# Performance work log

Hardware: AMD Instinct MI355X
Metric: run time of the kernel (lower is better)

## Reference

```python
import jax, jax.numpy as jnp
import numpy as np

N = 50000   # nodes
E = 800000  # edges
IN, HID, HEADS, OUT = 128, 32, 4, 64
NEG_SLOPE = 0.2


def _gatv2_layer(x, src, dst, Wl, bl, Wr, br, att, bias, res_W, concat):
    """One PyG-style GATv2Conv layer (eval mode, no dropout).
    x: [N, F_in]; att: [H, C]. Returns [N, H*C] if concat else [N, C]."""
    H, C = att.shape
    xl = (x @ Wl + bl).reshape(N, H, C)   # source transform
    xr = (x @ Wr + br).reshape(N, H, C)   # target transform
    e = jax.nn.leaky_relu(xl[src] + xr[dst], NEG_SLOPE)        # [E, H, C]
    logit = jnp.einsum('ehc,hc->eh', e, att)                   # [E, H]
    # segment softmax over incoming edges per destination node
    m = jax.ops.segment_max(logit, dst, num_segments=N)        # [N, H]
    p = jnp.exp(logit - m[dst])
    denom = jax.ops.segment_sum(p, dst, num_segments=N)
    alpha = p / (denom[dst] + 1e-16)                           # [E, H]
    out = jax.ops.segment_sum(xl[src] * alpha[:, :, None], dst, num_segments=N)  # [N, H, C]
    out = out.reshape(N, H * C) if concat else out.mean(axis=1)
    if res_W is not None:
        out = out + x @ res_W
    return out + bias


def _glorot(key, shape):
    fan_in = shape[0] if len(shape) > 1 else shape[-1]
    return jax.random.normal(key, shape, dtype=jnp.float32) / np.sqrt(fan_in)


def setup_inputs() -> dict:
    key = jax.random.key(0)
    ks = iter(jax.random.split(key, 32))
    x = jax.random.normal(next(ks), (N, IN), dtype=jnp.float32)
    edge_index = jax.random.randint(next(ks), (2, E), 0, N, dtype=jnp.int64)
    d = {"x": x, "edge_index": edge_index}
    HC = HEADS * HID  # 128
    # layer 0: IN -> HEADS*HID, concat, residual
    d["Wl0"] = _glorot(next(ks), (IN, HC)); d["bl0"] = jnp.zeros((HC,), jnp.float32)
    d["Wr0"] = _glorot(next(ks), (IN, HC)); d["br0"] = jnp.zeros((HC,), jnp.float32)
    d["att0"] = _glorot(next(ks), (HEADS, HID)); d["b0"] = jnp.zeros((HC,), jnp.float32)
    d["res0"] = _glorot(next(ks), (IN, HC))
    # layer 1: HC -> HEADS*HID, concat, residual
    d["Wl1"] = _glorot(next(ks), (HC, HC)); d["bl1"] = jnp.zeros((HC,), jnp.float32)
    d["Wr1"] = _glorot(next(ks), (HC, HC)); d["br1"] = jnp.zeros((HC,), jnp.float32)
    d["att1"] = _glorot(next(ks), (HEADS, HID)); d["b1"] = jnp.zeros((HC,), jnp.float32)
    d["res1"] = _glorot(next(ks), (HC, HC))
    # layer 2: HC -> OUT, heads=1, concat=False, no residual
    d["Wl2"] = _glorot(next(ks), (HC, OUT)); d["bl2"] = jnp.zeros((OUT,), jnp.float32)
    d["Wr2"] = _glorot(next(ks), (HC, OUT)); d["br2"] = jnp.zeros((OUT,), jnp.float32)
    d["att2"] = _glorot(next(ks), (1, OUT)); d["b2"] = jnp.zeros((OUT,), jnp.float32)
    return d


def reference(x, edge_index,
              Wl0, bl0, Wr0, br0, att0, b0, res0,
              Wl1, bl1, Wr1, br1, att1, b1, res1,
              Wl2, bl2, Wr2, br2, att2, b2):
    src, dst = edge_index[0], edge_index[1]
    h = _gatv2_layer(x, src, dst, Wl0, bl0, Wr0, br0, att0, b0, res0, True)
    h = jax.nn.elu(h)
    h = _gatv2_layer(h, src, dst, Wl1, bl1, Wr1, br1, att1, b1, res1, True)
    h = jax.nn.elu(h)
    return _gatv2_layer(h, src, dst, Wl2, bl2, Wr2, br2, att2, b2, None, False)
```

## Files before the change

kernel.cpp:

```cpp
#include <hip/hip_runtime.h>
#include <math.h>

#define NN 50000
#define EE 800000
#define NBK 196
#define EPB 4096

typedef short v8s __attribute__((ext_vector_type(8)));
typedef float v4f __attribute__((ext_vector_type(4)));
typedef float v16f __attribute__((ext_vector_type(16)));

__device__ __forceinline__ ushort f2bf(float f) {
    uint u = __float_as_uint(f);
    uint r = (u + 0x7fffu + ((u >> 16) & 1u)) >> 16;
    return (ushort)r;
}
__device__ __forceinline__ float bf2f(ushort h) {
    return __uint_as_float(((uint)h) << 16);
}
__device__ __forceinline__ float lrelu(float x) {
    return fmaf(0.4f, fabsf(x), 0.6f * x);
}

template <int CTRL>
__device__ __forceinline__ float dppadd(float x) {
    int y = __builtin_amdgcn_update_dpp(0, __float_as_int(x), CTRL, 0xf, 0xf, true);
    return x + __int_as_float(y);
}
__device__ __forceinline__ float sum8(float x) {
    x = dppadd<0xB1>(x);
    x = dppadd<0x4E>(x);
    x = dppadd<0x141>(x);
    return x;
}
__device__ __forceinline__ float sum16(float x) {
    x = sum8(x);
    x = dppadd<0x140>(x);
    return x;
}
__device__ __forceinline__ float expclamp(float t) {
    return __expf(fminf(fmaxf(t, -60.f), 80.f));
}

__global__ __launch_bounds__(256) void k_bktcnt(const int* __restrict__ edst,
                                                int* __restrict__ bcnt) {
    __shared__ int h[NBK];
    int t = threadIdx.x;
    if (t < NBK) h[t] = 0;
    __syncthreads();
    int eb = blockIdx.x * EPB;
    #pragma unroll
    for (int k = 0; k < EPB / 256; ++k) {
        int e = eb + k * 256 + t;
        if (e < EE) atomicAdd(&h[edst[e] >> 8], 1);
    }
    __syncthreads();
    if (t < NBK && h[t]) atomicAdd(&bcnt[t], h[t]);
}

__global__ __launch_bounds__(256) void k_bscan(const int* __restrict__ bcnt,
                                               int* __restrict__ bbase,
                                               int* __restrict__ bcur) {
    __shared__ int sm[256];
    int t = threadIdx.x;
    int v = (t < NBK) ? bcnt[t] : 0;
    sm[t] = v;
    __syncthreads();
    for (int o = 1; o < 256; o <<= 1) {
        int a = (t >= o) ? sm[t - o] : 0;
        __syncthreads();
        sm[t] += a;
        __syncthreads();
    }
    if (t < NBK) { int ex = sm[t] - v; bbase[t] = ex; bcur[t] = ex; }
}

__global__ __launch_bounds__(256) void k_bktplace(const int* __restrict__ esrc,
                                                  const int* __restrict__ edst,
                                                  int* __restrict__ bcur,
                                                  uint* __restrict__ ebuf) {
    __shared__ int h[NBK];
    __shared__ int base[NBK];
    int t = threadIdx.x;
    if (t < NBK) h[t] = 0;
    __syncthreads();
    int eb = blockIdx.x * EPB;
    int pk[EPB / 256];
    #pragma unroll
    for (int k = 0; k < EPB / 256; ++k) {
        int e = eb + k * 256 + t;
        pk[k] = -1;
        if (e < EE) {
            int b = edst[e] >> 8;
            int r = atomicAdd(&h[b], 1);
            pk[k] = (b << 16) | r;
        }
    }
    __syncthreads();
    if (t < NBK && h[t]) base[t] = atomicAdd(&bcur[t], h[t]);
    __syncthreads();
    #pragma unroll
    for (int k = 0; k < EPB / 256; ++k) {
        int e = eb + k * 256 + t;
        if (e < EE) {
            int b = pk[k] >> 16;
            int r = pk[k] & 0xFFFF;
            uint dl = (uint)(edst[e] & 255);
            ebuf[base[b] + r] = (dl << 16) | (uint)esrc[e];
        }
    }
}

__global__ __launch_bounds__(256) void k_bktfin(const uint* __restrict__ ebuf,
                                                const int* __restrict__ bbase,
                                                const int* __restrict__ bcnt,
                                                int* __restrict__ rowptr,
                                                int* __restrict__ csrc) {
    __shared__ int deg[256];
    __shared__ int sm[256];
    __shared__ int cur[256];
    const int b = blockIdx.x;
    const int t = threadIdx.x;
    const int eb = bbase[b];
    const int ec = bcnt[b];
    deg[t] = 0;
    __syncthreads();
    for (int k = t; k < ec; k += 256)
        atomicAdd(&deg[ebuf[eb + k] >> 16], 1);
    __syncthreads();
    int v = deg[t];
    sm[t] = v;
    __syncthreads();
    for (int o = 1; o < 256; o <<= 1) {
        int a = (t >= o) ? sm[t - o] : 0;
        __syncthreads();
        sm[t] += a;
        __syncthreads();
    }
    int node = b * 256 + t;
    if (node < NN) rowptr[node + 1] = eb + sm[t];
    if (node == 0) rowptr[0] = 0;
    cur[t] = sm[t] - v;
    __syncthreads();
    for (int k = t; k < ec; k += 256) {
        uint u = ebuf[eb + k];
        int nl = (int)(u >> 16);
        int r = atomicAdd(&cur[nl], 1);
        csrc[eb + r] = (int)(u & 0xFFFFu);
    }
}

struct WPack {
    const float* W[8];
    ushort* Th[8];
    ushort* Tl[8];
    int fout[8];
};

__global__ __launch_bounds__(256) void k_conv_w(WPack p) {
    int wi = blockIdx.y;
    int fout = p.fout[wi];
    int total = 128 * fout;
    int i = blockIdx.x * 256 + threadIdx.x;
    if (i >= total) return;
    int k = i / fout;
    int n = i - k * fout;
    float f = p.W[wi][i];
    ushort h = f2bf(f);
    float lo = f - bf2f(h);
    int t = n >> 5, c32 = n & 31, c = k >> 4, khalf = (k >> 3) & 1, j = k & 7;
    int flat = (((t * 8 + c) * 64) + khalf * 32 + c32) * 8 + j;
    p.Th[wi][flat] = h;
    p.Tl[wi][flat] = f2bf(lo);
}

template <int FOUT, int NW, bool CVT>
__global__ __launch_bounds__(128) void k_gemm_mfma(
    const float* __restrict__ Xf,
    const ushort* __restrict__ Xh, const ushort* __restrict__ Xl,
    const ushort* __restrict__ T0h, const ushort* __restrict__ T0l, const float* __restrict__ B0,
    const ushort* __restrict__ T1h, const ushort* __restrict__ T1l, const float* __restrict__ B1,
    const ushort* __restrict__ T2h, const ushort* __restrict__ T2l,
    ushort* __restrict__ O0b, float* __restrict__ O1, float* __restrict__ O2)
{
    const int lane  = threadIdx.x & 63;
    const int wid   = threadIdx.x >> 6;
    const int c32   = lane & 31;
    const int khalf = lane >> 5;
    const int row0  = blockIdx.x * 64 + wid * 32;

    const ushort* Th[3] = {T0h, T1h, T2h};
    const ushort* Tl[3] = {T0l, T1l, T2l};
    const float*  Bp[3] = {B0, B1, nullptr};

    v8s ah[8], al[8];
    {
        int arow = row0 + c32;
        if (arow > NN - 1) arow = NN - 1;
        #pragma unroll
        for (int c = 0; c < 8; ++c) {
            size_t off = (size_t)arow * 128 + c * 16 + khalf * 8;
            if constexpr (CVT) {
                float4 f0 = *(const float4*)(Xf + off);
                float4 f1 = *(const float4*)(Xf + off + 4);
                const float fe[8] = {f0.x, f0.y, f0.z, f0.w, f1.x, f1.y, f1.z, f1.w};
                #pragma unroll
                for (int e = 0; e < 8; ++e) {
                    ushort h = f2bf(fe[e]);
                    float lo = fe[e] - bf2f(h);
                    ah[c][e] = (short)h;
                    al[c][e] = (short)(__float_as_uint(lo) >> 16);
                }
            } else {
                ah[c] = *(const v8s*)(Xh + off);
                al[c] = *(const v8s*)(Xl + off);
            }
        }
    }

    #pragma unroll
    for (int w = 0; w < NW; ++w) {
        const ushort* th = Th[w];
        const ushort* tl = Tl[w];
        const float* bias = Bp[w];
        float* Of = (w == 1) ? O1 : O2;
        #pragma unroll
        for (int t = 0; t < FOUT / 32; ++t) {
            v16f acc = {0.f,0.f,0.f,0.f, 0.f,0.f,0.f,0.f, 0.f,0.f,0.f,0.f, 0.f,0.f,0.f,0.f};
            #pragma unroll
            for (int c = 0; c < 8; ++c) {
                int boff = ((t * 8 + c) * 64 + lane) * 8;
                v8s bh = *(const v8s*)(th + boff);
                v8s bl = *(const v8s*)(tl + boff);
                acc = __builtin_amdgcn_mfma_f32_32x32x16_bf16(al[c], bh, acc, 0, 0, 0);
                acc = __builtin_amdgcn_mfma_f32_32x32x16_bf16(ah[c], bl, acc, 0, 0, 0);
                acc = __builtin_amdgcn_mfma_f32_32x32x16_bf16(ah[c], bh, acc, 0, 0, 0);
            }
            const int col = t * 32 + c32;
            float badd = bias ? bias[col] : 0.f;
            if (w == 0) {
                #pragma unroll
                for (int reg = 0; reg < 16; ++reg) {
                    int r = row0 + (reg & 3) + 8 * (reg >> 2) + 4 * khalf;
                    if (r < NN) O0b[(size_t)r * FOUT + col] = f2bf(acc[reg] + badd);
                }
            } else {
                #pragma unroll
                for (int reg = 0; reg < 16; ++reg) {
                    int r = row0 + (reg & 3) + 8 * (reg >> 2) + 4 * khalf;
                    if (r < NN) Of[(size_t)r * FOUT + col] = acc[reg] + badd;
                }
            }
        }
    }
}

__global__ __launch_bounds__(256) void k_agg01(const ushort* __restrict__ XLb,
                                               const float4* __restrict__ XR4,
                                               const float4* __restrict__ RES4,
                                               const float* __restrict__ att,
                                               const float* __restrict__ bias,
                                               const int* __restrict__ rowptr,
                                               const int* __restrict__ csrc,
                                               ushort* __restrict__ Hh,
                                               ushort* __restrict__ Hl) {
    const int lane = threadIdx.x & 63;
    const int wid = threadIdx.x >> 6;
    const int n = blockIdx.x * 4 + wid;
    if (n >= NN) return;
    const int beg = rowptr[n];
    const int end = rowptr[n + 1];
    const int half = lane >> 5;
    const uint j = lane & 31;

    const float4 xr = XR4[(uint)n * 32u + j];
    const float4 at = ((const float4*)att)[j];
    float4 s = {0.f, 0.f, 0.f, 0.f};
    float d = 0.f;

    int i = beg;
    for (; i + 4 <= end; i += 4) {
        uint sa = (uint)csrc[i + half];
        uint sb = (uint)csrc[i + 2 + half];
        ushort4 ua = *(const ushort4*)(XLb + sa * 128u + 4u * j);
        ushort4 ub = *(const ushort4*)(XLb + sb * 128u + 4u * j);
        {
            float4 va = {bf2f(ua.x), bf2f(ua.y), bf2f(ua.z), bf2f(ua.w)};
            float t0 = lrelu(va.x + xr.x) * at.x;
            t0 = fmaf(lrelu(va.y + xr.y), at.y, t0);
            t0 = fmaf(lrelu(va.z + xr.z), at.z, t0);
            t0 = fmaf(lrelu(va.w + xr.w), at.w, t0);
            float p = expclamp(sum8(t0));
            d += p;
            s.x = fmaf(p, va.x, s.x); s.y = fmaf(p, va.y, s.y);
            s.z = fmaf(p, va.z, s.z); s.w = fmaf(p, va.w, s.w);
        }
        {
            float4 vb = {bf2f(ub.x), bf2f(ub.y), bf2f(ub.z), bf2f(ub.w)};
            float t0 = lrelu(vb.x + xr.x) * at.x;
            t0 = fmaf(lrelu(vb.y + xr.y), at.y, t0);
            t0 = fmaf(lrelu(vb.z + xr.z), at.z, t0);
            t0 = fmaf(lrelu(vb.w + xr.w), at.w, t0);
            float p = expclamp(sum8(t0));
            d += p;
            s.x = fmaf(p, vb.x, s.x); s.y = fmaf(p, vb.y, s.y);
            s.z = fmaf(p, vb.z, s.z); s.w = fmaf(p, vb.w, s.w);
        }
    }
    for (; i < end; i += 2) {
        int ia = i + half;
        if (ia > end - 1) ia = end - 1;
        uint sa = (uint)csrc[ia];
        ushort4 ua = *(const ushort4*)(XLb + sa * 128u + 4u * j);
        float4 va = {bf2f(ua.x), bf2f(ua.y), bf2f(ua.z), bf2f(ua.w)};
        float t0 = lrelu(va.x + xr.x) * at.x;
        t0 = fmaf(lrelu(va.y + xr.y), at.y, t0);
        t0 = fmaf(lrelu(va.z + xr.z), at.z, t0);
        t0 = fmaf(lrelu(va.w + xr.w), at.w, t0);
        float p = expclamp(sum8(t0));
        if (half && (i + 1 >= end)) p = 0.f;
        d += p;
        s.x = fmaf(p, va.x, s.x); s.y = fmaf(p, va.y, s.y);
        s.z = fmaf(p, va.z, s.z); s.w = fmaf(p, va.w, s.w);
    }

    d   += __shfl_xor(d, 32);
    s.x += __shfl_xor(s.x, 32);
    s.y += __shfl_xor(s.y, 32);
    s.z += __shfl_xor(s.z, 32);
    s.w += __shfl_xor(s.w, 32);

    if (half == 0) {
        float inv = (d > 0.f) ? 1.f / d : 0.f;
        float4 rv = RES4[(uint)n * 32u + j];
        float4 bv = ((const float4*)bias)[j];
        float o0 = fmaf(s.x, inv, rv.x + bv.x);
        float o1 = fmaf(s.y, inv, rv.y + bv.y);
        float o2 = fmaf(s.z, inv, rv.z + bv.z);
        float o3 = fmaf(s.w, inv, rv.w + bv.w);
        o0 = o0 > 0.f ? o0 : __expf(o0) - 1.f;
        o1 = o1 > 0.f ? o1 : __expf(o1) - 1.f;
        o2 = o2 > 0.f ? o2 : __expf(o2) - 1.f;
        o3 = o3 > 0.f ? o3 : __expf(o3) - 1.f;
        ushort4 h, l;
        h.x = f2bf(o0); l.x = f2bf(o0 - bf2f(h.x));
        h.y = f2bf(o1); l.y = f2bf(o1 - bf2f(h.y));
        h.z = f2bf(o2); l.z = f2bf(o2 - bf2f(h.z));
        h.w = f2bf(o3); l.w = f2bf(o3 - bf2f(h.w));
        *(ushort4*)(Hh + (uint)n * 128u + 4u * j) = h;
        *(ushort4*)(Hl + (uint)n * 128u + 4u * j) = l;
    }
}

__global__ __launch_bounds__(256) void k_agg2(const ushort* __restrict__ XLb,
                                              const float4* __restrict__ XR4,
                                              const float* __restrict__ att,
                                              const float* __restrict__ bias,
                                              const int* __restrict__ rowptr,
                                              const int* __restrict__ csrc,
                                              float* __restrict__ OUT) {
    const int lane = threadIdx.x & 63;
    const int wid = threadIdx.x >> 6;
    const int n = blockIdx.x * 4 + wid;
    if (n >= NN) return;
    const int beg = rowptr[n];
    const int end = rowptr[n + 1];
    const int q = lane >> 4;
    const uint jj = lane & 15;

    const float4 xr = XR4[(uint)n * 16u + jj];
    const float4 at = ((const float4*)att)[jj];
    float4 s = {0.f, 0.f, 0.f, 0.f};
    float d = 0.f;
    const int e1 = end - 1;

    for (int i = beg; i < end; i += 8) {
        int i0 = i + q;
        int i1 = i + 4 + q;
        uint s0 = (uint)csrc[min(i0, e1)];
        uint s1 = (uint)csrc[min(i1, e1)];
        ushort4 u0 = *(const ushort4*)(XLb + s0 * 64u + 4u * jj);
        ushort4 u1 = *(const ushort4*)(XLb + s1 * 64u + 4u * jj);
        #pragma unroll
        for (int u = 0; u < 2; ++u) {
            ushort4 uv = (u == 0) ? u0 : u1;
            int ii = (u == 0) ? i0 : i1;
            float4 v = {bf2f(uv.x), bf2f(uv.y), bf2f(uv.z), bf2f(uv.w)};
            float t0 = lrelu(v.x + xr.x) * at.x;
            t0 = fmaf(lrelu(v.y + xr.y), at.y, t0);
            t0 = fmaf(lrelu(v.z + xr.z), at.z, t0);
            t0 = fmaf(lrelu(v.w + xr.w), at.w, t0);
            float p = expclamp(sum16(t0));
            if (ii >= end) p = 0.f;
            d += p;
            s.x = fmaf(p, v.x, s.x); s.y = fmaf(p, v.y, s.y);
            s.z = fmaf(p, v.z, s.z); s.w = fmaf(p, v.w, s.w);
        }
    }

    d   += __shfl_xor(d, 16);   d   += __shfl_xor(d, 32);
    s.x += __shfl_xor(s.x, 16); s.x += __shfl_xor(s.x, 32);
    s.y += __shfl_xor(s.y, 16); s.y += __shfl_xor(s.y, 32);
    s.z += __shfl_xor(s.z, 16); s.z += __shfl_xor(s.z, 32);
    s.w += __shfl_xor(s.w, 16); s.w += __shfl_xor(s.w, 32);

    if (lane < 16) {
        float inv = (d > 0.f) ? 1.f / d : 0.f;
        float4 bv = ((const float4*)bias)[jj];
        float4 o;
        o.x = fmaf(s.x, inv, bv.x);
        o.y = fmaf(s.y, inv, bv.y);
        o.z = fmaf(s.z, inv, bv.z);
        o.w = fmaf(s.w, inv, bv.w);
        *(float4*)(OUT + (uint)n * 64u + 4u * jj) = o;
    }
}

extern "C" void kernel_launch(void* const* d_in, const int* in_sizes, int n_in,
                              void* d_out, int out_size, void* d_ws, size_t ws_size,
                              hipStream_t stream) {
    const float* x    = (const float*)d_in[0];
    const int*   ei   = (const int*)d_in[1];
    const int*   esrc = ei;
    const int*   edst = ei + EE;

    const float* Wl0 = (const float*)d_in[2];
    const float* bl0 = (const float*)d_in[3];
    const float* Wr0 = (const float*)d_in[4];
    const float* br0 = (const float*)d_in[5];
    const float* at0 = (const float*)d_in[6];
    const float* b0  = (const float*)d_in[7];
    const float* rs0 = (const float*)d_in[8];
    const float* Wl1 = (const float*)d_in[9];
    const float* bl1 = (const float*)d_in[10];
    const float* Wr1 = (const float*)d_in[11];
    const float* br1 = (const float*)d_in[12];
    const float* at1 = (const float*)d_in[13];
    const float* b1  = (const float*)d_in[14];
    const float* rs1 = (const float*)d_in[15];
    const float* Wl2 = (const float*)d_in[16];
    const float* bl2 = (const float*)d_in[17];
    const float* Wr2 = (const float*)d_in[18];
    const float* br2 = (const float*)d_in[19];
    const float* at2 = (const float*)d_in[20];
    const float* b2  = (const float*)d_in[21];

    float* out = (float*)d_out;

    ushort* XLb = (ushort*)d_ws;
    float* XR  = (float*)(XLb + (size_t)NN * 128);
    float* RES = XR + (size_t)NN * 128;
    ushort* Xh = (ushort*)(RES + (size_t)NN * 128);
    ushort* Xl_ = Xh + (size_t)NN * 128;
    ushort* Wth = Xl_ + (size_t)NN * 128;
    const int wsz[8] = {16384, 16384, 16384, 16384, 16384, 16384, 8192, 8192};
    ushort* th[8]; ushort* tl[8];
    {
        ushort* p = Wth;
        for (int i = 0; i < 8; ++i) { th[i] = p; p += wsz[i]; }
        for (int i = 0; i < 8; ++i) { tl[i] = p; p += wsz[i]; }
    }
    int* bcnt   = (int*)(Wth + 2 * (6 * 16384 + 2 * 8192));
    int* bbase  = bcnt + 256;
    int* bcur   = bbase + 256;
    int* rowptr = bcur + 256;
    int* csrc   = rowptr + (NN + 1);
    uint* ebuf  = (uint*)(csrc + EE);

    hipMemsetAsync(bcnt, 0, 256 * sizeof(int), stream);
    const int ebk = (EE + EPB - 1) / EPB;
    k_bktcnt<<<ebk, 256, 0, stream>>>(edst, bcnt);
    k_bscan<<<1, 256, 0, stream>>>(bcnt, bbase, bcur);
    k_bktplace<<<ebk, 256, 0, stream>>>(esrc, edst, bcur, ebuf);
    k_bktfin<<<NBK, 256, 0, stream>>>(ebuf, bbase, bcnt, rowptr, csrc);

    WPack wp;
    const float* Ws[8] = {Wl0, Wr0, rs0, Wl1, Wr1, rs1, Wl2, Wr2};
    const int fouts[8] = {128, 128, 128, 128, 128, 128, 64, 64};
    for (int i = 0; i < 8; ++i) { wp.W[i] = Ws[i]; wp.Th[i] = th[i]; wp.Tl[i] = tl[i]; wp.fout[i] = fouts[i]; }
    k_conv_w<<<dim3(64, 8), 256, 0, stream>>>(wp);

    const int gemm_gx = (NN + 63) / 64;
    const int agg_grid = (NN + 3) / 4;

    k_gemm_mfma<128, 3, true><<<gemm_gx, 128, 0, stream>>>(x, nullptr, nullptr,
        th[0], tl[0], bl0, th[1], tl[1], br0, th[2], tl[2], XLb, XR, RES);
    k_agg01<<<agg_grid, 256, 0, stream>>>(XLb, (const float4*)XR, (const float4*)RES,
        at0, b0, rowptr, csrc, Xh, Xl_);

    k_gemm_mfma<128, 3, false><<<gemm_gx, 128, 0, stream>>>(nullptr, Xh, Xl_,
        th[3], tl[3], bl1, th[4], tl[4], br1, th[5], tl[5], XLb, XR, RES);
    k_agg01<<<agg_grid, 256, 0, stream>>>(XLb, (const float4*)XR, (const float4*)RES,
        at1, b1, rowptr, csrc, Xh, Xl_);

    k_gemm_mfma<64, 2, false><<<gemm_gx, 128, 0, stream>>>(nullptr, Xh, Xl_,
        th[6], tl[6], bl2, th[7], tl[7], br2, nullptr, nullptr, XLb, XR, nullptr);
    k_agg2<<<agg_grid, 256, 0, stream>>>(XLb, (const float4*)XR, at2, b2, rowptr, csrc, out);
}
```

Before: 381.4 us.

## Fuse CSR build launches with weight conversion and shrink GEMM blocks to one wave

Merges the bucket-count kernel and the weight bf16 split-conversion into one launch, and removes the separate scan kernel. Each place and finalize block now recomputes the 196-entry bucket prefix scan itself. This cuts the preprocessing chain from five launches to three and removes serialization between them, at the cost of redundant scan work in every block. The GEMM kernels also switch to 64-thread blocks covering 32 rows each, doubling the grid, for finer scheduling granularity.

```diff
diff --git a/kernel.cpp b/kernel.cpp
--- a/kernel.cpp
+++ b/kernel.cpp
@@ -42,48 +42,71 @@
     return __expf(fminf(fmaxf(t, -60.f), 80.f));
 }
 
-__global__ __launch_bounds__(256) void k_bktcnt(const int* __restrict__ edst,
-                                                int* __restrict__ bcnt) {
-    __shared__ int h[NBK];
+struct WPack {
+    const float* W[8];
+    ushort* Th[8];
+    ushort* Tl[8];
+    int fout[8];
+};
+
+__global__ __launch_bounds__(256) void k_build1(const int* __restrict__ edst,
+                                                int* __restrict__ bcnt,
+                                                WPack p) {
     int t = threadIdx.x;
-    if (t < NBK) h[t] = 0;
-    __syncthreads();
-    int eb = blockIdx.x * EPB;
-    #pragma unroll
-    for (int k = 0; k < EPB / 256; ++k) {
-        int e = eb + k * 256 + t;
-        if (e < EE) atomicAdd(&h[edst[e] >> 8], 1);
-    }
-    __syncthreads();
-    if (t < NBK && h[t]) atomicAdd(&bcnt[t], h[t]);
-}
-
-__global__ __launch_bounds__(256) void k_bscan(const int* __restrict__ bcnt,
-                                               int* __restrict__ bbase,
-                                               int* __restrict__ bcur) {
-    __shared__ int sm[256];
-    int t = threadIdx.x;
-    int v = (t < NBK) ? bcnt[t] : 0;
-    sm[t] = v;
-    __syncthreads();
-    for (int o = 1; o < 256; o <<= 1) {
-        int a = (t >= o) ? sm[t - o] : 0;
-        __syncthreads();
-        sm[t] += a;
-        __syncthreads();
-    }
-    if (t < NBK) { int ex = sm[t] - v; bbase[t] = ex; bcur[t] = ex; }
+    if (blockIdx.x < 196) {
+        __shared__ int h[NBK];
+        if (t < NBK) h[t] = 0;
+        __syncthreads();
+        int eb = blockIdx.x * EPB;
+        #pragma unroll
+        for (int k = 0; k < EPB / 256; ++k) {
+            int e = eb + k * 256 + t;
+            if (e < EE) atomicAdd(&h[edst[e] >> 8], 1);
+        }
+        __syncthreads();
+        if (t < NBK && h[t]) atomicAdd(&bcnt[t], h[t]);
+    } else {
+        int bid = blockIdx.x - 196;
+        int wi = bid >> 6;
+        int ib = bid & 63;
+        int fout = p.fout[wi];
+        int total = 128 * fout;
+        int i = ib * 256 + t;
+        if (i >= total) return;
+        int k = i / fout;
+        int n = i - k * fout;
+        float f = p.W[wi][i];
+        ushort h = f2bf(f);
+        float lo = f - bf2f(h);
+        int tt = n >> 5, c32 = n & 31, c = k >> 4, khalf = (k >> 3) & 1, j = k & 7;
+        int flat = (((tt * 8 + c) * 64) + khalf * 32 + c32) * 8 + j;
+        p.Th[wi][flat] = h;
+        p.Tl[wi][flat] = f2bf(lo);
+    }
 }
 
 __global__ __launch_bounds__(256) void k_bktplace(const int* __restrict__ esrc,
                                                   const int* __restrict__ edst,
-                                                  int* __restrict__ bcur,
+                                                  const int* __restrict__ bcnt,
+                                                  int* __restrict__ gcur,
                                                   uint* __restrict__ ebuf) {
+    __shared__ int sc[256];
     __shared__ int h[NBK];
     __shared__ int base[NBK];
     int t = threadIdx.x;
+    int v = (t < NBK) ? bcnt[t] : 0;
+    sc[t] = v;
+    __syncthreads();
+    for (int o = 1; o < 256; o <<= 1) {
+        int a = (t >= o) ? sc[t - o] : 0;
+        __syncthreads();
+        sc[t] += a;
+        __syncthreads();
+    }
+    int bexcl = sc[t] - v;
     if (t < NBK) h[t] = 0;
     __syncthreads();
+
     int eb = blockIdx.x * EPB;
     int pk[EPB / 256];
     #pragma unroll
@@ -97,7 +120,7 @@
         }
     }
     __syncthreads();
-    if (t < NBK && h[t]) base[t] = atomicAdd(&bcur[t], h[t]);
+    if (t < NBK && h[t]) base[t] = bexcl + atomicAdd(&gcur[t], h[t]);
     __syncthreads();
     #pragma unroll
     for (int k = 0; k < EPB / 256; ++k) {
@@ -112,24 +135,36 @@
 }
 
 __global__ __launch_bounds__(256) void k_bktfin(const uint* __restrict__ ebuf,
-                                                const int* __restrict__ bbase,
                                                 const int* __restrict__ bcnt,
                                                 int* __restrict__ rowptr,
                                                 int* __restrict__ csrc) {
+    __shared__ int sm[256];
     __shared__ int deg[256];
-    __shared__ int sm[256];
     __shared__ int cur[256];
+    __shared__ int s_eb, s_ec;
     const int b = blockIdx.x;
     const int t = threadIdx.x;
-    const int eb = bbase[b];
-    const int ec = bcnt[b];
+
+    int v = (t < NBK) ? bcnt[t] : 0;
+    sm[t] = v;
     deg[t] = 0;
     __syncthreads();
+    for (int o = 1; o < 256; o <<= 1) {
+        int a = (t >= o) ? sm[t - o] : 0;
+        __syncthreads();
+        sm[t] += a;
+        __syncthreads();
+    }
+    if (t == b) { s_eb = sm[t] - v; s_ec = v; }
+    __syncthreads();
+    const int eb = s_eb;
+    const int ec = s_ec;
+
     for (int k = t; k < ec; k += 256)
         atomicAdd(&deg[ebuf[eb + k] >> 16], 1);
     __syncthreads();
-    int v = deg[t];
-    sm[t] = v;
+    int dv = deg[t];
+    sm[t] = dv;
     __syncthreads();
     for (int o = 1; o < 256; o <<= 1) {
         int a = (t >= o) ? sm[t - o] : 0;
@@ -140,7 +175,7 @@
     int node = b * 256 + t;
     if (node < NN) rowptr[node + 1] = eb + sm[t];
     if (node == 0) rowptr[0] = 0;
-    cur[t] = sm[t] - v;
+    cur[t] = sm[t] - dv;
     __syncthreads();
     for (int k = t; k < ec; k += 256) {
         uint u = ebuf[eb + k];
@@ -150,32 +185,8 @@
     }
 }
 
-struct WPack {
-    const float* W[8];
-    ushort* Th[8];
-    ushort* Tl[8];
-    int fout[8];
-};
-
-__global__ __launch_bounds__(256) void k_conv_w(WPack p) {
-    int wi = blockIdx.y;
-    int fout = p.fout[wi];
-    int total = 128 * fout;
-    int i = blockIdx.x * 256 + threadIdx.x;
-    if (i >= total) return;
-    int k = i / fout;
-    int n = i - k * fout;
-    float f = p.W[wi][i];
-    ushort h = f2bf(f);
-    float lo = f - bf2f(h);
-    int t = n >> 5, c32 = n & 31, c = k >> 4, khalf = (k >> 3) & 1, j = k & 7;
-    int flat = (((t * 8 + c) * 64) + khalf * 32 + c32) * 8 + j;
-    p.Th[wi][flat] = h;
-    p.Tl[wi][flat] = f2bf(lo);
-}
-
 template <int FOUT, int NW, bool CVT>
-__global__ __launch_bounds__(128) void k_gemm_mfma(
+__global__ __launch_bounds__(64) void k_gemm_mfma(
     const float* __restrict__ Xf,
     const ushort* __restrict__ Xh, const ushort* __restrict__ Xl,
     const ushort* __restrict__ T0h, const ushort* __restrict__ T0l, const float* __restrict__ B0,
@@ -184,10 +195,9 @@
     ushort* __restrict__ O0b, float* __restrict__ O1, float* __restrict__ O2)
 {
     const int lane  = threadIdx.x & 63;
-    const int wid   = threadIdx.x >> 6;
     const int c32   = lane & 31;
     const int khalf = lane >> 5;
-    const int row0  = blockIdx.x * 64 + wid * 32;
+    const int row0  = blockIdx.x * 32;
 
     const ushort* Th[3] = {T0h, T1h, T2h};
     const ushort* Tl[3] = {T0l, T1l, T2l};
@@ -461,39 +471,35 @@
         for (int i = 0; i < 8; ++i) { tl[i] = p; p += wsz[i]; }
     }
     int* bcnt   = (int*)(Wth + 2 * (6 * 16384 + 2 * 8192));
-    int* bbase  = bcnt + 256;
-    int* bcur   = bbase + 256;
-    int* rowptr = bcur + 256;
+    int* gcur   = bcnt + 256;
+    int* rowptr = gcur + 256;
     int* csrc   = rowptr + (NN + 1);
     uint* ebuf  = (uint*)(csrc + EE);
-
-    hipMemsetAsync(bcnt, 0, 256 * sizeof(int), stream);
-    const int ebk = (EE + EPB - 1) / EPB;
-    k_bktcnt<<<ebk, 256, 0, stream>>>(edst, bcnt);
-    k_bscan<<<1, 256, 0, stream>>>(bcnt, bbase, bcur);
-    k_bktplace<<<ebk, 256, 0, stream>>>(esrc, edst, bcur, ebuf);
-    k_bktfin<<<NBK, 256, 0, stream>>>(ebuf, bbase, bcnt, rowptr, csrc);
 
     WPack wp;
     const float* Ws[8] = {Wl0, Wr0, rs0, Wl1, Wr1, rs1, Wl2, Wr2};
     const int fouts[8] = {128, 128, 128, 128, 128, 128, 64, 64};
     for (int i = 0; i < 8; ++i) { wp.W[i] = Ws[i]; wp.Th[i] = th[i]; wp.Tl[i] = tl[i]; wp.fout[i] = fouts[i]; }
-    k_conv_w<<<dim3(64, 8), 256, 0, stream>>>(wp);
-
-    const int gemm_gx = (NN + 63) / 64;
+
+    hipMemsetAsync(bcnt, 0, 512 * sizeof(int), stream);
+    k_build1<<<196 + 512, 256, 0, stream>>>(edst, bcnt, wp);
+    k_bktplace<<<196, 256, 0, stream>>>(esrc, edst, bcnt, gcur, ebuf);
+    k_bktfin<<<NBK, 256, 0, stream>>>(ebuf, bcnt, rowptr, csrc);
+
+    const int gemm_gx = (NN + 31) / 32;
     const int agg_grid = (NN + 3) / 4;
 
-    k_gemm_mfma<128, 3, true><<<gemm_gx, 128, 0, stream>>>(x, nullptr, nullptr,
+    k_gemm_mfma<128, 3, true><<<gemm_gx, 64, 0, stream>>>(x, nullptr, nullptr,
         th[0], tl[0], bl0, th[1], tl[1], br0, th[2], tl[2], XLb, XR, RES);
     k_agg01<<<agg_grid, 256, 0, stream>>>(XLb, (const float4*)XR, (const float4*)RES,
         at0, b0, rowptr, csrc, Xh, Xl_);
 
-    k_gemm_mfma<128, 3, false><<<gemm_gx, 128, 0, stream>>>(nullptr, Xh, Xl_,
+    k_gemm_mfma<128, 3, false><<<gemm_gx, 64, 0, stream>>>(nullptr, Xh, Xl_,
         th[3], tl[3], bl1, th[4], tl[4], br1, th[5], tl[5], XLb, XR, RES);
     k_agg01<<<agg_grid, 256, 0, stream>>>(XLb, (const float4*)XR, (const float4*)RES,
         at1, b1, rowptr, csrc, Xh, Xl_);
 
-    k_gemm_mfma<64, 2, false><<<gemm_gx, 128, 0, stream>>>(nullptr, Xh, Xl_,
+    k_gemm_mfma<64, 2, false><<<gemm_gx, 64, 0, stream>>>(nullptr, Xh, Xl_,
         th[6], tl[6], bl2, th[7], tl[7], br2, nullptr, nullptr, XLb, XR, nullptr);
     k_agg2<<<agg_grid, 256, 0, stream>>>(XLb, (const float4*)XR, at2, b2, rowptr, csrc, out);
 }
```

Measured after the change: 375.6 us. About the same (-1.5%).
